# Performance work log

Measured on AMD Instinct MI355X. Metric: run time of the kernel, lower is better.

The kernel has to match this reference:

```python
import jax, jax.numpy as jnp
import numpy as np


def _make_grid(h, w):
    """Replicates gen_grid_coordinates_optimized(h, w, stride=1) vectorized in numpy.
    Returns (h*3, w*3, 2) float32 grid in grid_sample convention (x=col, y=row, in [-1,1])."""
    pi = np.pi
    dphi = pi / h
    dtheta = 2 * pi / w
    tp, tt, icp = np.tan(dphi), np.tan(dtheta), 1.0 / np.cos(dphi)
    xys = np.array([[(-tt, icp * tp), (0, tp), (tt, icp * tp)],
                    [(-tt, 0), (1, 1), (tt, 0)],
                    [(-tt, -icp * tp), (0, -tp), (tt, -icp * tp)]], dtype=np.float64)
    xk, yk = xys[..., 0], xys[..., 1]          # (3,3) kernel offsets on tangent plane
    rho = np.sqrt(xk ** 2 + yk ** 2)
    v = np.arctan(rho)
    cv, sv = np.cos(v), np.sin(v)
    rr = np.arange(h, dtype=np.float64)
    cc = np.arange(w, dtype=np.float64)
    phi = -((rr + 0.5) / h * pi - pi / 2)      # (h,)
    theta = (cc + 0.5) / w * 2 * pi - pi       # (w,)
    cph = np.cos(phi)[:, None, None]
    sph = np.sin(phi)[:, None, None]
    # (h,3,3) ; clip guards fp roundoff at poles (mathematically |arg|<=1)
    new_phi = np.arcsin(np.clip(cv * sph + yk * sv * cph / rho, -1.0, 1.0))
    dtheta_off = np.arctan(xk * sv / (rho * cph * cv - yk * sph * sv))  # (h,3,3)
    new_theta = theta[None, :, None, None] + dtheta_off[:, None]        # (h,w,3,3)
    new_r = np.broadcast_to(((-new_phi + pi / 2) * h / pi - 0.5)[:, None], (h, w, 3, 3)).copy()
    new_c = (new_theta + pi) * w / (2 * pi) - 0.5
    new_c = (new_c + w) % w
    # kernel center samples the pixel itself
    new_r[:, :, 1, 1] = rr[:, None]
    new_c[:, :, 1, 1] = cc[None, :]
    gy = new_r * 2 / h - 1
    gx = new_c * 2 / w - 1
    grid = np.stack([gx, gy], axis=-1)                      # (h,w,ki,kj,2)
    grid = grid.transpose(0, 2, 1, 3, 4).reshape(h * 3, w * 3, 2)
    return grid.astype(np.float32)


def _grid_sample_bilinear(x, grid):
    """F.grid_sample(mode='bilinear', align_corners=True, padding_mode='zeros').
    x: (N,C,H,W), grid: (Hg,Wg,2) shared across batch. Returns (N,C,Hg,Wg)."""
    N, C, H, W = x.shape
    ix = (grid[..., 0] + 1) * 0.5 * (W - 1)
    iy = (grid[..., 1] + 1) * 0.5 * (H - 1)
    x0 = jnp.floor(ix)
    y0 = jnp.floor(iy)
    x1, y1 = x0 + 1, y0 + 1
    xflat = x.reshape(N, C, H * W)

    def corner(yc, xc, wgt):
        valid = (xc >= 0) & (xc <= W - 1) & (yc >= 0) & (yc <= H - 1)
        xi = jnp.clip(xc, 0, W - 1).astype(jnp.int32)
        yi = jnp.clip(yc, 0, H - 1).astype(jnp.int32)
        idx = (yi * W + xi).reshape(-1)
        v = xflat[:, :, idx].reshape(N, C, *xc.shape)
        return v * (wgt * valid)[None, None]

    out = (corner(y0, x0, (x1 - ix) * (y1 - iy))
           + corner(y0, x1, (ix - x0) * (y1 - iy))
           + corner(y1, x0, (x1 - ix) * (iy - y0))
           + corner(y1, x1, (ix - x0) * (iy - y0)))
    return out


def setup_inputs() -> dict:
    key = jax.random.key(0)
    k1, k2 = jax.random.split(key)
    B, Cin, Cout, H, W = 4, 16, 32, 256, 512
    x = jax.random.normal(k1, (B, Cin, H, W), dtype=jnp.float32)
    fan_out = Cout * 9  # kaiming_normal fan_out, relu gain
    weight = jax.random.normal(k2, (Cout, Cin, 3, 3), dtype=jnp.float32) * np.sqrt(2.0 / fan_out)
    bias = jnp.zeros((Cout,), dtype=jnp.float32)
    grid = jnp.asarray(_make_grid(H, W))  # (H*3, W*3, 2) constant spherical warp
    return {"x": x, "weight": weight, "bias": bias, "grid": grid}


def reference(x, weight, bias, grid):
    s = _grid_sample_bilinear(x, grid)  # (N,C,3H,3W)
    out = jax.lax.conv_general_dilated(
        s, weight, window_strides=(3, 3), padding='VALID',
        dimension_numbers=('NCHW', 'OIHW', 'NCHW'))
    return out + bias[None, :, None, None]
```

## Files before the change

### kernel.cpp

```cpp
#include <hip/hip_runtime.h>

#define HH 256
#define WW 512
#define NCIN 16
#define NCOUT 32
#define NB 4

typedef _Float16 half8 __attribute__((ext_vector_type(8)));
typedef float f32x16 __attribute__((ext_vector_type(16)));

#define XT_OFF   0u
#define XTAB_OFF 16777216u
#define WFRAG_OFF (16777216u + 9437184u)
#define YTAB_OFF (16777216u + 9437184u + 16384u)
#define WS_NEED  (YTAB_OFF + 36864u)

__global__ __launch_bounds__(256) void precompute_all(const float* __restrict__ x,
                                                      const float* __restrict__ w,
                                                      const float* __restrict__ grid,
                                                      _Float16* __restrict__ xh,
                                                      float2* __restrict__ xtab,
                                                      _Float16* __restrict__ wfrag,
                                                      float4* __restrict__ ytab) {
    const float2* g2 = reinterpret_cast<const float2*>(grid);
    if (blockIdx.x < 2048) {
        const int lb = (blockIdx.x & 7) * 256 + (blockIdx.x >> 3);
        const int t = lb * 256 + threadIdx.x;
        const int c = t & (WW - 1);
        const int r = (t >> 9) & (HH - 1);
        const int b = t >> 17;
        const float* xp = x + ((size_t)(b * NCIN) * HH + r) * WW + c;
        half8 h0, h1;
#pragma unroll
        for (int ci = 0; ci < 8; ++ci)  h0[ci] = (_Float16)xp[(size_t)ci * (HH * WW)];
#pragma unroll
        for (int ci = 0; ci < 8; ++ci)  h1[ci] = (_Float16)xp[(size_t)(8 + ci) * (HH * WW)];
        half8* op = reinterpret_cast<half8*>(xh) + (size_t)t * 2;
        op[0] = h0;
        op[1] = h1;
        return;
    }
    if (blockIdx.x < 6656) {
        const int T = (blockIdx.x - 2048) * 256 + threadIdx.x;
        const int gr = T / 1536, j = T - gr * 1536;
        const int r = gr / 3, kr = gr - r * 3;
        const int c = j / 3, kc = j - c * 3;
        const float gx = g2[(size_t)gr * 1536 + j].x;
        const float ix = ((gx + 1.0f) * 0.5f) * (float)(WW - 1);
        const float x0f = floorf(ix);
        xtab[(size_t)(r * 9 + kr * 3 + kc) * WW + c] = make_float2(ix - x0f, __int_as_float((int)x0f));
        return;
    }
    if (blockIdx.x < 6674) {
        const int e = (blockIdx.x - 6656) * 256 + threadIdx.x;
        const int j = e & 7, lane = (e >> 3) & 63, t = e >> 9;
        const int c32 = lane & 31, h = lane >> 5;
        wfrag[e] = (_Float16)w[c32 * 144 + (h * 8 + j) * 9 + t];
        return;
    }
    const int u = (blockIdx.x - 6674) * 256 + threadIdx.x;
    if (u < HH * 9) {
        const int r = u / 9, tap = u - r * 9;
        const int kr = tap / 3, kc = tap - kr * 3;
        const float gy = g2[(size_t)(r * 3 + kr) * 1536 + kc].y;
        const float iy = ((gy + 1.0f) * 0.5f) * (float)(HH - 1);
        const float y0f = floorf(iy);
        const float fy = iy - y0f;
        const int y0 = (int)y0f, y1 = y0 + 1;
        float wy0 = 1.0f - fy, wy1 = fy;
        if (y0 < 0 || y0 > HH - 1) wy0 = 0.0f;
        if (y1 < 0 || y1 > HH - 1) wy1 = 0.0f;
        const int cy0 = min(max(y0, 0), HH - 1), cy1 = min(max(y1, 0), HH - 1);
        ytab[u] = make_float4(wy0, wy1, __int_as_float(cy0), __int_as_float(cy1));
    }
}

__global__ __launch_bounds__(256, 4) void sphere_mfma_kernel(const _Float16* __restrict__ xh,
                                                             const float2* __restrict__ xtab,
                                                             const _Float16* __restrict__ wfrag,
                                                             const float4* __restrict__ ytab,
                                                             const float* __restrict__ bias,
                                                             float* __restrict__ out) {
    const int tid = threadIdx.x, lane = tid & 63, wv = tid >> 6;
    const int c32 = lane & 31, h = lane >> 5;
    const int px = wv * 32 + c32;

    const int lb = ((blockIdx.x & 7) << 9) + (blockIdx.x >> 3);
    const int pixbase = lb << 7;
    const int b    = pixbase >> 17;
    const int rimg = (pixbase >> 9) & (HH - 1);
    const int c0   = pixbase & (WW - 1);

    float wy0s[9], wy1s[9];
    int Rb0[9], Rb1[9];
#pragma unroll
    for (int t = 0; t < 9; ++t) {
        const float4 y = ytab[rimg * 9 + t];
        wy0s[t] = y.x;
        wy1s[t] = y.y;
        Rb0[t] = (b * HH + __float_as_int(y.z)) << 10;
        Rb1[t] = (b * HH + __float_as_int(y.w)) << 10;
    }

    const float2* xrow = xtab + (size_t)rimg * 9 * WW + (c0 + px);
    float2 f2s[9];
#pragma unroll
    for (int t = 0; t < 9; ++t) f2s[t] = xrow[t * WW];

    const half8* wf8 = reinterpret_cast<const half8*>(wfrag);
    half8 wA[9];
#pragma unroll
    for (int t = 0; t < 9; ++t) wA[t] = wf8[t * 64 + lane];

    const half8* x8 = reinterpret_cast<const half8*>(xh);
    f32x16 acc = {};

    half8 A00a, A01a, A10a, A11a, A00b, A01b, A10b, A11b;

#define GLOAD(tt, S)                                                     \
    {                                                                    \
        const int x0_ = __float_as_int(f2s[tt].y);                       \
        const int p0_ = Rb0[tt] + (x0_ << 1) + h;                        \
        const int p1_ = Rb1[tt] + (x0_ << 1) + h;                        \
        A00##S = x8[p0_];                                                \
        A01##S = x8[p0_ + 2];                                            \
        A10##S = x8[p1_];                                                \
        A11##S = x8[p1_ + 2];                                            \
    }

#define CONSUME(tt, S)                                                   \
    {                                                                    \
        const float fx_ = f2s[tt].x;                                     \
        const float wx0_ = 1.0f - fx_;                                   \
        const float w00_ = wx0_ * wy0s[tt], w01_ = fx_ * wy0s[tt];       \
        const float w10_ = wx0_ * wy1s[tt], w11_ = fx_ * wy1s[tt];       \
        const _Float16 W00_ = (_Float16)w00_, W01_ = (_Float16)w01_;     \
        const _Float16 W10_ = (_Float16)w10_, W11_ = (_Float16)w11_;     \
        const half8 B00_ = {W00_, W00_, W00_, W00_, W00_, W00_, W00_, W00_}; \
        const half8 B01_ = {W01_, W01_, W01_, W01_, W01_, W01_, W01_, W01_}; \
        const half8 B10_ = {W10_, W10_, W10_, W10_, W10_, W10_, W10_, W10_}; \
        const half8 B11_ = {W11_, W11_, W11_, W11_, W11_, W11_, W11_, W11_}; \
        half8 pk_ = A00##S * B00_;                                       \
        pk_ += A01##S * B01_;                                            \
        pk_ += A10##S * B10_;                                            \
        pk_ += A11##S * B11_;                                            \
        acc = __builtin_amdgcn_mfma_f32_32x32x16_f16(wA[tt], pk_, acc, 0, 0, 0); \
    }

    GLOAD(0, a)
    GLOAD(1, b)
    CONSUME(0, a) GLOAD(2, a)
    CONSUME(1, b) GLOAD(3, b)
    CONSUME(2, a) GLOAD(4, a)
    CONSUME(3, b) GLOAD(5, b)
    CONSUME(4, a) GLOAD(6, a)
    CONSUME(5, b) GLOAD(7, b)
    CONSUME(6, a) GLOAD(8, a)
    CONSUME(7, b)
    CONSUME(8, a)
#undef GLOAD
#undef CONSUME

    const int pix = c0 + wv * 32 + c32;
    float* ob = out + (((size_t)(b * NCOUT) * HH + rimg) * WW) + pix;
#pragma unroll
    for (int reg = 0; reg < 16; ++reg) {
        const int co = (reg & 3) + 8 * (reg >> 2) + 4 * h;
        ob[(size_t)co * (HH * WW)] = acc[reg] + bias[co];
    }
}

__global__ __launch_bounds__(256) void sphere_conv_fallback(const float* __restrict__ x,
                                                            const float* __restrict__ weight,
                                                            const float* __restrict__ bias,
                                                            const float* __restrict__ grid,
                                                            float* __restrict__ out) {
    __shared__ float wlds[NCIN * 9 * NCOUT];
    const int tid = threadIdx.x;
    for (int e = tid; e < NCIN * 9 * NCOUT; e += 256) {
        const int co  = e & (NCOUT - 1);
        const int cik = e >> 5;
        wlds[e] = weight[co * (NCIN * 9) + cik];
    }
    __syncthreads();

    const int pindex = blockIdx.x * 256 + tid;
    const int c = pindex & (WW - 1);
    const int r = (pindex >> 9) & (HH - 1);
    const int b = pindex >> 17;

    float acc[NCOUT];
#pragma unroll
    for (int o = 0; o < NCOUT; ++o) acc[o] = 0.0f;

    const float2* g2 = reinterpret_cast<const float2*>(grid);

#pragma unroll 1
    for (int k = 0; k < 9; ++k) {
        const int kr = k / 3, kc = k - kr * 3;
        const float2 g = g2[(r * 3 + kr) * (WW * 3) + (c * 3 + kc)];
        const float ix = ((g.x + 1.0f) * 0.5f) * (float)(WW - 1);
        const float iy = ((g.y + 1.0f) * 0.5f) * (float)(HH - 1);
        const float x0f = floorf(ix), y0f = floorf(iy);
        const float fx = ix - x0f, fy = iy - y0f;
        const int x0 = (int)x0f, y0 = (int)y0f;
        const int x1 = x0 + 1, y1 = y0 + 1;
        float wx0 = 1.0f - fx, wx1 = fx, wy0 = 1.0f - fy, wy1 = fy;
        if (x0 < 0 || x0 > WW - 1) wx0 = 0.0f;
        if (x1 < 0 || x1 > WW - 1) wx1 = 0.0f;
        if (y0 < 0 || y0 > HH - 1) wy0 = 0.0f;
        if (y1 < 0 || y1 > HH - 1) wy1 = 0.0f;
        const int cx0 = min(max(x0, 0), WW - 1), cx1 = min(max(x1, 0), WW - 1);
        const int cy0 = min(max(y0, 0), HH - 1), cy1 = min(max(y1, 0), HH - 1);
        const float w00 = wx0 * wy0, w01 = wx1 * wy0, w10 = wx0 * wy1, w11 = wx1 * wy1;

#pragma unroll 1
        for (int ci = 0; ci < NCIN; ++ci) {
            const float* xb = x + (size_t)((b * NCIN + ci) * HH) * WW;
            const float a00 = xb[cy0 * WW + cx0];
            const float a01 = xb[cy0 * WW + cx1];
            const float a10 = xb[cy1 * WW + cx0];
            const float a11 = xb[cy1 * WW + cx1];
            const float s = w00 * a00 + w01 * a01 + w10 * a10 + w11 * a11;
            const float4* wl = reinterpret_cast<const float4*>(&wlds[(ci * 9 + k) * NCOUT]);
#pragma unroll
            for (int o = 0; o < 8; ++o) {
                const float4 wv = wl[o];
                acc[o * 4 + 0] += wv.x * s;
                acc[o * 4 + 1] += wv.y * s;
                acc[o * 4 + 2] += wv.z * s;
                acc[o * 4 + 3] += wv.w * s;
            }
        }
    }

    const int obase = ((b * NCOUT) * HH + r) * WW + c;
#pragma unroll
    for (int o = 0; o < NCOUT; ++o) {
        out[obase + o * (HH * WW)] = acc[o] + bias[o];
    }
}

extern "C" void kernel_launch(void* const* d_in, const int* in_sizes, int n_in,
                              void* d_out, int out_size, void* d_ws, size_t ws_size,
                              hipStream_t stream) {
    const float* x    = (const float*)d_in[0];
    const float* w    = (const float*)d_in[1];
    const float* bias = (const float*)d_in[2];
    const float* grid = (const float*)d_in[3];
    float* out = (float*)d_out;

    if (ws_size >= WS_NEED) {
        char* ws = (char*)d_ws;
        _Float16* xh    = (_Float16*)(ws + XT_OFF);
        float2*   xtab  = (float2*)(ws + XTAB_OFF);
        _Float16* wfrag = (_Float16*)(ws + WFRAG_OFF);
        float4*   ytab  = (float4*)(ws + YTAB_OFF);

        precompute_all<<<6683, 256, 0, stream>>>(x, w, grid, xh, xtab, wfrag, ytab);
        sphere_mfma_kernel<<<4096, 256, 0, stream>>>(xh, xtab, wfrag, ytab, bias, out);
    } else {
        sphere_conv_fallback<<<2048, 256, 0, stream>>>(x, w, bias, grid, out);
    }
}
```

Baseline: 49.78 us.

## Stage gathered fp16 corners through LDS with triple-buffered direct global-to-LDS loads

```diff
diff --git a/kernel.cpp b/kernel.cpp
--- a/kernel.cpp
+++ b/kernel.cpp
@@ -8,6 +8,9 @@
 
 typedef _Float16 half8 __attribute__((ext_vector_type(8)));
 typedef float f32x16 __attribute__((ext_vector_type(16)));
+
+typedef const __attribute__((address_space(1))) void gvoid_t;
+typedef __attribute__((address_space(3))) void lvoid_t;
 
 #define XT_OFF   0u
 #define XTAB_OFF 16777216u
@@ -75,12 +78,13 @@
     }
 }
 
-__global__ __launch_bounds__(256, 4) void sphere_mfma_kernel(const _Float16* __restrict__ xh,
-                                                             const float2* __restrict__ xtab,
-                                                             const _Float16* __restrict__ wfrag,
-                                                             const float4* __restrict__ ytab,
-                                                             const float* __restrict__ bias,
-                                                             float* __restrict__ out) {
+__global__ __launch_bounds__(256) void sphere_mfma_kernel(const _Float16* __restrict__ xh,
+                                                          const float2* __restrict__ xtab,
+                                                          const _Float16* __restrict__ wfrag,
+                                                          const float4* __restrict__ ytab,
+                                                          const float* __restrict__ bias,
+                                                          float* __restrict__ out) {
+    __shared__ _Float16 Sl[4][3][4][512];
     const int tid = threadIdx.x, lane = tid & 63, wv = tid >> 6;
     const int c32 = lane & 31, h = lane >> 5;
     const int px = wv * 32 + c32;
@@ -112,53 +116,62 @@
 #pragma unroll
     for (int t = 0; t < 9; ++t) wA[t] = wf8[t * 64 + lane];
 
-    const half8* x8 = reinterpret_cast<const half8*>(xh);
+    const char* xbase = reinterpret_cast<const char*>(xh);
     f32x16 acc = {};
 
-    half8 A00a, A01a, A10a, A11a, A00b, A01b, A10b, A11b;
-
-#define GLOAD(tt, S)                                                     \
-    {                                                                    \
-        const int x0_ = __float_as_int(f2s[tt].y);                       \
-        const int p0_ = Rb0[tt] + (x0_ << 1) + h;                        \
-        const int p1_ = Rb1[tt] + (x0_ << 1) + h;                        \
-        A00##S = x8[p0_];                                                \
-        A01##S = x8[p0_ + 2];                                            \
-        A10##S = x8[p1_];                                                \
-        A11##S = x8[p1_ + 2];                                            \
-    }
-
-#define CONSUME(tt, S)                                                   \
-    {                                                                    \
-        const float fx_ = f2s[tt].x;                                     \
-        const float wx0_ = 1.0f - fx_;                                   \
-        const float w00_ = wx0_ * wy0s[tt], w01_ = fx_ * wy0s[tt];       \
-        const float w10_ = wx0_ * wy1s[tt], w11_ = fx_ * wy1s[tt];       \
-        const _Float16 W00_ = (_Float16)w00_, W01_ = (_Float16)w01_;     \
-        const _Float16 W10_ = (_Float16)w10_, W11_ = (_Float16)w11_;     \
-        const half8 B00_ = {W00_, W00_, W00_, W00_, W00_, W00_, W00_, W00_}; \
-        const half8 B01_ = {W01_, W01_, W01_, W01_, W01_, W01_, W01_, W01_}; \
-        const half8 B10_ = {W10_, W10_, W10_, W10_, W10_, W10_, W10_, W10_}; \
-        const half8 B11_ = {W11_, W11_, W11_, W11_, W11_, W11_, W11_, W11_}; \
-        half8 pk_ = A00##S * B00_;                                       \
-        pk_ += A01##S * B01_;                                            \
-        pk_ += A10##S * B10_;                                            \
-        pk_ += A11##S * B11_;                                            \
-        acc = __builtin_amdgcn_mfma_f32_32x32x16_f16(wA[tt], pk_, acc, 0, 0, 0); \
-    }
-
-    GLOAD(0, a)
-    GLOAD(1, b)
-    CONSUME(0, a) GLOAD(2, a)
-    CONSUME(1, b) GLOAD(3, b)
-    CONSUME(2, a) GLOAD(4, a)
-    CONSUME(3, b) GLOAD(5, b)
-    CONSUME(4, a) GLOAD(6, a)
-    CONSUME(5, b) GLOAD(7, b)
-    CONSUME(6, a) GLOAD(8, a)
-    CONSUME(7, b)
-    CONSUME(8, a)
-#undef GLOAD
+#define ISSUE(tt)                                                                 \
+    {                                                                             \
+        const int x0_ = __float_as_int(f2s[tt].y);                                \
+        const size_t p0_ = (size_t)(unsigned)(Rb0[tt] + (x0_ << 1) + h) << 4;     \
+        const size_t p1_ = (size_t)(unsigned)(Rb1[tt] + (x0_ << 1) + h) << 4;     \
+        __builtin_amdgcn_global_load_lds((gvoid_t*)(xbase + p0_),                 \
+                                         (lvoid_t*)&Sl[wv][(tt) % 3][0][0], 16, 0, 0); \
+        __builtin_amdgcn_global_load_lds((gvoid_t*)(xbase + p0_ + 32),            \
+                                         (lvoid_t*)&Sl[wv][(tt) % 3][1][0], 16, 0, 0); \
+        __builtin_amdgcn_global_load_lds((gvoid_t*)(xbase + p1_),                 \
+                                         (lvoid_t*)&Sl[wv][(tt) % 3][2][0], 16, 0, 0); \
+        __builtin_amdgcn_global_load_lds((gvoid_t*)(xbase + p1_ + 32),            \
+                                         (lvoid_t*)&Sl[wv][(tt) % 3][3][0], 16, 0, 0); \
+    }
+
+#define CONSUME(tt, VM)                                                           \
+    {                                                                             \
+        asm volatile("s_waitcnt vmcnt(" VM ")" ::: "memory");                     \
+        __builtin_amdgcn_sched_barrier(0);                                        \
+        const half8 A00 = *reinterpret_cast<const half8*>(&Sl[wv][(tt) % 3][0][lane * 8]); \
+        const half8 A01 = *reinterpret_cast<const half8*>(&Sl[wv][(tt) % 3][1][lane * 8]); \
+        const half8 A10 = *reinterpret_cast<const half8*>(&Sl[wv][(tt) % 3][2][lane * 8]); \
+        const half8 A11 = *reinterpret_cast<const half8*>(&Sl[wv][(tt) % 3][3][lane * 8]); \
+        const float fx_ = f2s[tt].x;                                              \
+        const float wx0_ = 1.0f - fx_;                                            \
+        const float w00_ = wx0_ * wy0s[tt], w01_ = fx_ * wy0s[tt];                \
+        const float w10_ = wx0_ * wy1s[tt], w11_ = fx_ * wy1s[tt];                \
+        const _Float16 W00_ = (_Float16)w00_, W01_ = (_Float16)w01_;              \
+        const _Float16 W10_ = (_Float16)w10_, W11_ = (_Float16)w11_;              \
+        const half8 B00_ = {W00_, W00_, W00_, W00_, W00_, W00_, W00_, W00_};      \
+        const half8 B01_ = {W01_, W01_, W01_, W01_, W01_, W01_, W01_, W01_};      \
+        const half8 B10_ = {W10_, W10_, W10_, W10_, W10_, W10_, W10_, W10_};      \
+        const half8 B11_ = {W11_, W11_, W11_, W11_, W11_, W11_, W11_, W11_};      \
+        half8 pk_ = A00 * B00_;                                                   \
+        pk_ += A01 * B01_;                                                        \
+        pk_ += A10 * B10_;                                                        \
+        pk_ += A11 * B11_;                                                        \
+        acc = __builtin_amdgcn_mfma_f32_32x32x16_f16(wA[tt], pk_, acc, 0, 0, 0);  \
+    }
+
+    ISSUE(0)
+    ISSUE(1)
+    ISSUE(2)
+    CONSUME(0, "8") ISSUE(3)
+    CONSUME(1, "8") ISSUE(4)
+    CONSUME(2, "8") ISSUE(5)
+    CONSUME(3, "8") ISSUE(6)
+    CONSUME(4, "8") ISSUE(7)
+    CONSUME(5, "8") ISSUE(8)
+    CONSUME(6, "8")
+    CONSUME(7, "4")
+    CONSUME(8, "0")
+#undef ISSUE
 #undef CONSUME
 
     const int pix = c0 + wv * 32 + c32;
```

Result: no change. 50.38 us (+1.2%).
